# Optimization experiments

Hardware: AMD Instinct MI355X
Metric: run time of the kernel (lower is better)

The kernel has to match this reference:

```python
import jax, jax.numpy as jnp
import numpy as np

DIM = 1024
S_SIZE = 512
M_SIZE = 4096
L_SIZE = 8192
MERGE_THRESHOLD = 0.98
L_ALPHA = 0.1
K_PROMOTE = max(1, S_SIZE // 4)  # torch: min(len(candidates), max(1, s_size//4)); candidates >> s_size here


def _l2norm(x, axis=-1):
    # F.normalize(p=2) with eps clamp
    return x / jnp.maximum(jnp.linalg.norm(x, axis=axis, keepdims=True), 1e-12)


def _update(processed_tokens, s_memory, m_memory, l_memory, m_utility, l_utility, wq, bq, wk, bk, s_ptr):
    cand = processed_tokens.reshape(-1, DIM)
    # --- S tier: scatter top-k-norm candidates into ring buffer (vectorized; K<=S so slots distinct) ---
    norms = jnp.linalg.norm(cand, axis=1)
    _, top_idx = jax.lax.top_k(norms, K_PROMOTE)
    pos = (s_ptr + jnp.arange(K_PROMOTE)) % S_SIZE
    s_mem = s_memory.at[pos].set(cand[top_idx])
    s_ptr_new = (s_ptr + K_PROMOTE) % S_SIZE
    # --- promotion attention (1 head, only attn weights used): pick best short-term slot ---
    q = l_memory.mean(axis=0) @ wq.T + bq                      # [dim]
    kproj = s_mem @ wk.T + bk                                  # [S, dim]
    attn = jax.nn.softmax(kproj @ q / jnp.sqrt(jnp.asarray(DIM, cand.dtype)))
    best_s_idx = jnp.argmax(attn)
    candidate = s_mem[best_s_idx]                              # [dim]

    # --- M tier: promote / merge / replace ---
    def not_full(mm, mu):
        ridx = jnp.argmin(mu)
        return mm.at[ridx].set(candidate), mu.at[ridx].set(mu.mean() + 1e-5)

    def full(mm, mu):
        mm_norm = _l2norm(mm)
        sims = mm_norm @ _l2norm(candidate)                    # [M]
        msi = jnp.argmax(sims)
        sim_cand = sims[msi]

        def merge_with_candidate(mm, mu):
            merged = _l2norm((mm[msi] + candidate) / 2.0)
            return mm.at[msi].set(merged), mu.at[msi].set((mu[msi] + mu.mean()) / 2.0)

        def try_internal_merge(mm, mu):
            # most redundant pair: strict lower triangle of cosine sim matrix
            sim_mat = mm_norm @ mm_norm.T                      # [M, M]
            sim_mat = jnp.where(jnp.triu(jnp.ones((M_SIZE, M_SIZE), bool)), -1.0, sim_mat)
            flat = jnp.argmax(sim_mat)
            internal_sim = sim_mat.reshape(-1)[flat]
            idx1, idx2 = flat // M_SIZE, flat % M_SIZE

            def do_pair_merge(mm, mu):
                merged = _l2norm((mm[idx1] + mm[idx2]) / 2.0)
                mm2 = mm.at[idx1].set(merged).at[idx2].set(candidate)
                mu1 = mu.at[idx1].set((mu[idx1] + mu[idx2]) / 2.0)
                mu2 = mu1.at[idx2].set(mu1.mean() + 1e-5)      # torch recomputes mean after idx1 write
                return mm2, mu2

            def replace_weakest(mm, mu):
                li = jnp.argmin(mu)
                stronger = jnp.linalg.norm(candidate) > jnp.linalg.norm(mm[li])
                mm2 = jnp.where(stronger, mm.at[li].set(candidate), mm)
                mu2 = jnp.where(stronger, mu.at[li].set(mu.mean() + 1e-5), mu)
                return mm2, mu2

            return jax.lax.cond(internal_sim > MERGE_THRESHOLD, do_pair_merge, replace_weakest, mm, mu)

        return jax.lax.cond(sim_cand > MERGE_THRESHOLD, merge_with_candidate, try_internal_merge, mm, mu)

    is_m_full = ~jnp.any(m_utility == 0)
    m_mem, m_util = jax.lax.cond(is_m_full, full, not_full, m_memory, m_utility)
    # --- L tier: consolidate most-used M slot into least-used L slot ---
    mi = jnp.argmax(m_util)
    lj = jnp.argmin(l_utility)
    consolidated = (1.0 - L_ALPHA) * l_memory[lj] + L_ALPHA * m_mem[mi]
    l_mem = l_memory.at[lj].set(consolidated)
    l_util = l_utility.at[lj].set(l_utility.mean())            # mean of pre-write values
    return s_mem, m_mem, l_mem, m_util, l_util, s_ptr_new


def setup_inputs() -> dict:
    key = jax.random.key(0)
    ks = jax.random.split(key, 10)
    scale = 1.0 / np.sqrt(DIM)
    return {
        "processed_tokens": jax.random.normal(ks[0], (4, 4096, DIM), jnp.float32),
        "s_memory": jax.random.normal(ks[1], (S_SIZE, DIM), jnp.float32),
        "m_memory": jax.random.normal(ks[2], (M_SIZE, DIM), jnp.float32),
        "l_memory": jax.random.normal(ks[3], (L_SIZE, DIM), jnp.float32),
        "m_utility": jax.random.uniform(ks[4], (M_SIZE,), jnp.float32) + 0.01,  # >0 -> 'm full' branch
        "l_utility": jax.random.uniform(ks[5], (L_SIZE,), jnp.float32) + 0.01,
        "wq": jax.random.normal(ks[6], (DIM, DIM), jnp.float32) * scale,
        "bq": jnp.zeros((DIM,), jnp.float32),
        "wk": jax.random.normal(ks[7], (DIM, DIM), jnp.float32) * scale,
        "bk": jnp.zeros((DIM,), jnp.float32),
        "s_ptr": 0,
    }


def reference(processed_tokens, s_memory, m_memory, l_memory, m_utility, l_utility, wq, bq, wk, bk, s_ptr):
    return _update(processed_tokens, s_memory, m_memory, l_memory, m_utility, l_utility, wq, bq, wk, bk, s_ptr)
```

## Files before the change

### kernel.cpp

```cpp
#include <hip/hip_runtime.h>

#define DIMV 1024
#define SSZ 512
#define MSZ 4096
#define LSZ 8192
#define KPROM 128
#define NCAND 16384
#define NPAIR 528

typedef __attribute__((ext_vector_type(4))) float f32x4;
typedef __attribute__((ext_vector_type(4))) unsigned int u32x4;
typedef __attribute__((ext_vector_type(4))) unsigned short u16x4;
typedef __attribute__((ext_vector_type(8))) __bf16 bf16x8;

#define OUT_S 0ull
#define OUT_M 524288ull
#define OUT_L 4718592ull
#define OUT_MU 13107200ull
#define OUT_LU 13111296ull
#define OUT_SPTR 13119488ull

#define SCROWS 2080
#define SC_BF16 0ull
#define SC_NORMS 2097152ull
#define SC_TOPIDX 2113536ull
#define SC_RV 2113664ull
#define SC_LSUM 2114688ull
#define SC_QV 2115712ull
#define SC_LOGITS 2116736ull
#define SC_BEST 2117248ull
#define SC_MNORM 2117264ull
#define SC_SIMS 2121360ull
#define SC_PPV 2125456ull
#define SC_PPI 2125984ull

__device__ __forceinline__ float wave_sum(float v) {
#pragma unroll
  for (int o = 32; o > 0; o >>= 1) v += __shfl_down(v, o, 64);
  return v;
}
__device__ __forceinline__ void wave_maxidx(float& v, int& i) {
#pragma unroll
  for (int o = 32; o > 0; o >>= 1) {
    float ov = __shfl_down(v, o, 64);
    int oi = __shfl_down(i, o, 64);
    if (ov > v || (ov == v && oi < i)) { v = ov; i = oi; }
  }
}
__device__ __forceinline__ void wave_minidx(float& v, int& i) {
#pragma unroll
  for (int o = 32; o > 0; o >>= 1) {
    float ov = __shfl_down(v, o, 64);
    int oi = __shfl_down(i, o, 64);
    if (ov < v || (ov == v && oi < i)) { v = ov; i = oi; }
  }
}
__device__ __forceinline__ unsigned short f2bf(float x) {
  unsigned u = __float_as_uint(x);
  return (unsigned short)((u + 0x7FFFu + ((u >> 16) & 1u)) >> 16);
}
__device__ __forceinline__ void nts(f32x4* p, f32x4 v) { __builtin_nontemporal_store(v, p); }
__device__ __forceinline__ void gload16(const unsigned short* g, unsigned short* l) {
  __builtin_amdgcn_global_load_lds((const __attribute__((address_space(1))) unsigned int*)(g),
                                   (__attribute__((address_space(3))) unsigned int*)(l), 16, 0, 0);
}

__global__ void kA(const float* __restrict__ cand, const float* __restrict__ l_memory,
                   const float* __restrict__ m, float* __restrict__ norms,
                   float* __restrict__ lsum, unsigned short* __restrict__ mb,
                   float* __restrict__ mnorm, float* __restrict__ out_m,
                   float* __restrict__ out_l) {
  int b = blockIdx.x, t = threadIdx.x, lane = t & 63, w = t >> 6;
  if (b < 256) {
    int r0 = b * 32;
    const f32x4* base = (const f32x4*)l_memory + (size_t)r0 * 256;
    f32x4* dst = (f32x4*)out_l + (size_t)r0 * 256;
    bool wr = (r0 >= SCROWS);
    f32x4 a0 = {0.f, 0.f, 0.f, 0.f}, a1 = a0, a2 = a0, a3 = a0;
#pragma unroll 2
    for (int r = 0; r < 32; r += 4) {
      f32x4 v0 = base[(r + 0) * 256 + t];
      f32x4 v1 = base[(r + 1) * 256 + t];
      f32x4 v2 = base[(r + 2) * 256 + t];
      f32x4 v3 = base[(r + 3) * 256 + t];
      if (wr) {
        nts(&dst[(r + 0) * 256 + t], v0);
        nts(&dst[(r + 1) * 256 + t], v1);
        nts(&dst[(r + 2) * 256 + t], v2);
        nts(&dst[(r + 3) * 256 + t], v3);
      }
      a0 += v0; a1 += v1; a2 += v2; a3 += v3;
    }
    f32x4 a = (a0 + a1) + (a2 + a3);
    atomicAdd(&lsum[t * 4 + 0], a.x);
    atomicAdd(&lsum[t * 4 + 1], a.y);
    atomicAdd(&lsum[t * 4 + 2], a.z);
    atomicAdd(&lsum[t * 4 + 3], a.w);
  } else if (b < 512) {
    int r0 = (b - 256) * 16 + w * 4;
    const f32x4* base4 = (const f32x4*)(m + (size_t)r0 * DIMV);
    u16x4* mb4 = (u16x4*)(mb + (size_t)r0 * DIMV);
    f32x4* om4 = (f32x4*)(out_m + (size_t)r0 * DIMV);
    float s0 = 0.f, s1 = 0.f, s2 = 0.f, s3 = 0.f;
#pragma unroll
    for (int k = 0; k < 16; ++k) {
      int i = k * 64 + lane;
      f32x4 v = base4[i];
      float d = v.x * v.x + v.y * v.y + v.z * v.z + v.w * v.w;
      if (k < 4) s0 += d;
      else if (k < 8) s1 += d;
      else if (k < 12) s2 += d;
      else s3 += d;
      u16x4 h;
      h.x = f2bf(v.x); h.y = f2bf(v.y); h.z = f2bf(v.z); h.w = f2bf(v.w);
      mb4[i] = h;
      nts(&om4[i], v);
    }
    f32x4 sv = {s0, s1, s2, s3};
#pragma unroll
    for (int o = 32; o > 0; o >>= 1) {
      sv.x += __shfl_down(sv.x, o, 64);
      sv.y += __shfl_down(sv.y, o, 64);
      sv.z += __shfl_down(sv.z, o, 64);
      sv.w += __shfl_down(sv.w, o, 64);
    }
    if (lane == 0) {
      f32x4 o4 = {sqrtf(sv.x), sqrtf(sv.y), sqrtf(sv.z), sqrtf(sv.w)};
      *((f32x4*)(mnorm + r0)) = o4;
    }
  } else {
    int r0 = (b - 512) * 16 + w * 4;
    const f32x4* base4 = (const f32x4*)(cand + (size_t)r0 * DIMV);
    float s0 = 0.f, s1 = 0.f, s2 = 0.f, s3 = 0.f;
#pragma unroll
    for (int k = 0; k < 16; ++k) {
      f32x4 v = base4[k * 64 + lane];
      float d = v.x * v.x + v.y * v.y + v.z * v.z + v.w * v.w;
      if (k < 4) s0 += d;
      else if (k < 8) s1 += d;
      else if (k < 12) s2 += d;
      else s3 += d;
    }
    f32x4 sv = {s0, s1, s2, s3};
#pragma unroll
    for (int o = 32; o > 0; o >>= 1) {
      sv.x += __shfl_down(sv.x, o, 64);
      sv.y += __shfl_down(sv.y, o, 64);
      sv.z += __shfl_down(sv.z, o, 64);
      sv.w += __shfl_down(sv.w, o, 64);
    }
    if (lane == 0) {
      f32x4 o4 = {sqrtf(sv.x), sqrtf(sv.y), sqrtf(sv.z), sqrtf(sv.w)};
      *((f32x4*)(norms + r0)) = o4;
    }
  }
}

__device__ int scan_excl_1024(int v, int* sh, int* total) {
  int t = threadIdx.x;
  sh[t] = v;
  __syncthreads();
  for (int o = 1; o < 1024; o <<= 1) {
    int x = (t >= o) ? sh[t - o] : 0;
    __syncthreads();
    sh[t] += x;
    __syncthreads();
  }
  int incl = sh[t];
  *total = sh[1023];
  __syncthreads();
  return incl - v;
}

__global__ void kT(const float* __restrict__ norms, int* __restrict__ topidx) {
  int t = threadIdx.x;
  __shared__ int sh[1024];
  __shared__ int hist[256];
  __shared__ unsigned s_selkey[KPROM];
  __shared__ int s_selidx[KPROM];
  __shared__ int s_digit, s_sub;
  unsigned key[16];
  {
    const u32x4* np = (const u32x4*)norms;
    u32x4 k0 = np[t * 4 + 0], k1 = np[t * 4 + 1], k2 = np[t * 4 + 2], k3 = np[t * 4 + 3];
    key[0] = k0.x; key[1] = k0.y; key[2] = k0.z; key[3] = k0.w;
    key[4] = k1.x; key[5] = k1.y; key[6] = k1.z; key[7] = k1.w;
    key[8] = k2.x; key[9] = k2.y; key[10] = k2.z; key[11] = k2.w;
    key[12] = k3.x; key[13] = k3.y; key[14] = k3.z; key[15] = k3.w;
  }

  unsigned prefix = 0, himask = 0;
  int remaining = KPROM;
  for (int p = 24; p >= 0; p -= 8) {
    if (t < 256) hist[t] = 0;
    __syncthreads();
#pragma unroll
    for (int j = 0; j < 16; ++j)
      if ((key[j] & himask) == prefix) atomicAdd(&hist[(key[j] >> p) & 255], 1);
    __syncthreads();
    if (t < 256) sh[t] = hist[t];
    __syncthreads();
    for (int o = 1; o < 256; o <<= 1) {
      int x = (t < 256 && t + o < 256) ? sh[t + o] : 0;
      __syncthreads();
      if (t < 256) sh[t] += x;
      __syncthreads();
    }
    if (t < 256) {
      int sfex = (t < 255) ? sh[t + 1] : 0;
      if (sfex < remaining && remaining <= sh[t]) { s_digit = t; s_sub = sfex; }
    }
    __syncthreads();
    prefix |= ((unsigned)s_digit) << p;
    remaining -= s_sub;
    himask |= (0xFFu << p);
    __syncthreads();
  }
  unsigned T = prefix;

  int cgt = 0, ceq = 0;
#pragma unroll
  for (int j = 0; j < 16; ++j) { cgt += (key[j] > T); ceq += (key[j] == T); }
  int total_gt, total_eq;
  int sgt = scan_excl_1024(cgt, sh, &total_gt);
  int seq = scan_excl_1024(ceq, sh, &total_eq);
  int need_eq = KPROM - total_gt;
  int g = sgt, e = seq;
#pragma unroll
  for (int j = 0; j < 16; ++j) {
    if (key[j] > T) { s_selkey[g] = key[j]; s_selidx[g] = t * 16 + j; ++g; }
    else if (key[j] == T) {
      if (e < need_eq) { s_selkey[total_gt + e] = key[j]; s_selidx[total_gt + e] = t * 16 + j; }
      ++e;
    }
  }
  __syncthreads();
  if (t < KPROM) {
    unsigned mk = s_selkey[t];
    int mi = s_selidx[t];
    int rank = 0;
    for (int q2 = 0; q2 < KPROM; ++q2) {
      unsigned qk = s_selkey[q2];
      int qi = s_selidx[q2];
      rank += (qk > mk || (qk == mk && qi < mi)) ? 1 : 0;
    }
    topidx[rank] = mi;
  }
}

__global__ void kB(const float* __restrict__ cand, const float* __restrict__ s_memory,
                   const int* __restrict__ topidx, const int* __restrict__ s_ptr,
                   const float* __restrict__ wq, const float* __restrict__ bq,
                   const float* __restrict__ lsum, float* __restrict__ out_s,
                   float* __restrict__ out_sptr, float* __restrict__ qv) {
  int b = blockIdx.x, t = threadIdx.x;
  if (b < 512) {
    int sp = s_ptr[0];
    int k = (b - sp + SSZ) & (SSZ - 1);
    const float* src = (k < KPROM) ? (cand + (size_t)topidx[k] * DIMV) : (s_memory + (size_t)b * DIMV);
    ((f32x4*)(out_s + (size_t)b * DIMV))[t] = ((const f32x4*)src)[t];
    if (b == 0 && t == 0) out_sptr[0] = (float)((sp + KPROM) % SSZ);
  } else {
    int lane = t & 63, w = t >> 6;
    int d = (b - 512) * 4 + w;
    const f32x4* row = (const f32x4*)(wq + (size_t)d * DIMV);
    const f32x4* lm = (const f32x4*)lsum;
    float s = 0.f;
#pragma unroll
    for (int c = 0; c < 4; ++c) {
      f32x4 a = row[c * 64 + lane], bb = lm[c * 64 + lane];
      s += a.x * bb.x + a.y * bb.y + a.z * bb.z + a.w * bb.w;
    }
    s = wave_sum(s);
    if (lane == 0) qv[d] = s * (1.f / 8192.f) + bq[d];
  }
}

__global__ void kC(const float* __restrict__ wk, const float* __restrict__ qv,
                   float* __restrict__ rv) {
  int b = blockIdx.x, t = threadIdx.x;
  f32x4 a = {0.f, 0.f, 0.f, 0.f};
  for (int r = 0; r < 8; ++r) {
    float qd = qv[b * 8 + r];
    f32x4 v = ((const f32x4*)(wk + (size_t)(b * 8 + r) * DIMV))[t];
    a += v * qd;
  }
  atomicAdd(&rv[t * 4 + 0], a.x);
  atomicAdd(&rv[t * 4 + 1], a.y);
  atomicAdd(&rv[t * 4 + 2], a.z);
  atomicAdd(&rv[t * 4 + 3], a.w);
}

__global__ void kD(const float* __restrict__ out_s, const float* __restrict__ rv,
                   float* __restrict__ logits) {
  int lane = threadIdx.x & 63, w = threadIdx.x >> 6;
  int srow = blockIdx.x * 4 + w;
  const f32x4* a = (const f32x4*)(out_s + (size_t)srow * DIMV);
  const f32x4* b = (const f32x4*)rv;
  float s = 0.f;
#pragma unroll
  for (int c = 0; c < 4; ++c) {
    f32x4 x = a[c * 64 + lane], y = b[c * 64 + lane];
    s += x.x * y.x + x.y * y.y + x.z * y.z + x.w * y.w;
  }
  s = wave_sum(s);
  if (lane == 0) logits[srow] = s;
}

__global__ void kE(const float* __restrict__ logits, const float* __restrict__ out_s,
                   int* __restrict__ best, float* __restrict__ cnorm) {
  __shared__ float swv[4];
  __shared__ int swi[4];
  int t = threadIdx.x, lane = t & 63, w = t >> 6;
  float v0 = logits[t], v1 = logits[t + 256];
  float bv;
  int bidx;
  if (v1 > v0) { bv = v1; bidx = t + 256; } else { bv = v0; bidx = t; }
  wave_maxidx(bv, bidx);
  if (lane == 0) { swv[w] = bv; swi[w] = bidx; }
  __syncthreads();
  if (t == 0) {
    float a = swv[0]; int ai = swi[0];
    for (int i = 1; i < 4; ++i)
      if (swv[i] > a || (swv[i] == a && swi[i] < ai)) { a = swv[i]; ai = swi[i]; }
    best[0] = ai;
  }
  __syncthreads();
  int bi = best[0];
  f32x4 c4 = ((const f32x4*)(out_s + (size_t)bi * DIMV))[t];
  float s = c4.x * c4.x + c4.y * c4.y + c4.z * c4.z + c4.w * c4.w;
  s = wave_sum(s);
  __syncthreads();
  if (lane == 0) swv[w] = s;
  __syncthreads();
  if (t == 0) cnorm[0] = sqrtf(swv[0] + swv[1] + swv[2] + swv[3]);
}

__global__ __launch_bounds__(256, 3) void kG(const unsigned short* __restrict__ mb,
                                             const float* __restrict__ mnorm,
                                             const float* __restrict__ m,
                                             const float* __restrict__ out_s,
                                             const int* __restrict__ best,
                                             const float* __restrict__ cnorm,
                                             float* __restrict__ pv, int* __restrict__ pidx,
                                             float* __restrict__ sims) {
  int b = blockIdx.x, t = threadIdx.x, lane = t & 63, w = t >> 6;
  if (b >= NPAIR) {
    int row = (b - NPAIR) * 4 + w;
    const f32x4* mp = (const f32x4*)(m + (size_t)row * DIMV);
    const f32x4* cp = (const f32x4*)(out_s + (size_t)best[0] * DIMV);
    float sd = 0.f;
#pragma unroll
    for (int c = 0; c < 4; ++c) {
      int i = c * 64 + lane;
      f32x4 v = mp[i], u = cp[i];
      sd += v.x * u.x + v.y * u.y + v.z * u.z + v.w * u.w;
    }
    sd = wave_sum(sd);
    if (lane == 0) sims[row] = sd / (fmaxf(mnorm[row], 1e-12f) * fmaxf(cnorm[0], 1e-12f));
    return;
  }
  __shared__ unsigned short Ash[128 * 64];
  __shared__ unsigned short Bsh[128 * 64];
  __shared__ float spv[4];
  __shared__ int spi[4];

  int bs = (b & 7) * 66 + (b >> 3);
  int bi = (int)((sqrtf(8.f * (float)bs + 1.f) - 1.f) * 0.5f);
  while (bi * (bi + 1) / 2 > bs) --bi;
  while ((bi + 1) * (bi + 2) / 2 <= bs) ++bi;
  int bj = bs - bi * (bi + 1) / 2;
  int rowA0 = bi * 128, rowB0 = bj * 128;

  int wr = w >> 1, wc = w & 1;
  int rl = lane & 15, kq4 = lane >> 4;
  int swz = rl & 7;
  int subrow = lane >> 3, gg = lane & 7;
  int gsw = (gg ^ subrow) << 3;

  f32x4 acc[4][4];
  f32x4 z = {0.f, 0.f, 0.f, 0.f};
#pragma unroll
  for (int ti = 0; ti < 4; ++ti)
#pragma unroll
    for (int tj = 0; tj < 4; ++tj) acc[ti][tj] = z;

  for (int kc = 0; kc < DIMV; kc += 64) {
#pragma unroll
    for (int jj = 0; jj < 4; ++jj) {
      int rsub = w * 32 + jj * 8 + subrow;
      gload16(mb + (size_t)(rowA0 + rsub) * DIMV + kc + gsw, Ash + (w * 4 + jj) * 512);
      gload16(mb + (size_t)(rowB0 + rsub) * DIMV + kc + gsw, Bsh + (w * 4 + jj) * 512);
    }
    __syncthreads();
#pragma unroll
    for (int ks = 0; ks < 2; ++ks) {
      int co = (((ks * 4 + kq4) ^ swz) << 3);
      bf16x8 af[4], bfv[4];
#pragma unroll
      for (int ti = 0; ti < 4; ++ti)
        af[ti] = *(const bf16x8*)(Ash + (wr * 64 + ti * 16 + rl) * 64 + co);
#pragma unroll
      for (int tj = 0; tj < 4; ++tj)
        bfv[tj] = *(const bf16x8*)(Bsh + (wc * 64 + tj * 16 + rl) * 64 + co);
#pragma unroll
      for (int ti = 0; ti < 4; ++ti)
#pragma unroll
        for (int tj = 0; tj < 4; ++tj)
          acc[ti][tj] = __builtin_amdgcn_mfma_f32_16x16x32_bf16(af[ti], bfv[tj], acc[ti][tj], 0, 0, 0);
    }
    __syncthreads();
  }

  float ni[16], nj4[4];
#pragma unroll
  for (int ti = 0; ti < 4; ++ti)
#pragma unroll
    for (int r = 0; r < 4; ++r)
      ni[ti * 4 + r] = fmaxf(mnorm[rowA0 + wr * 64 + ti * 16 + kq4 * 4 + r], 1e-12f);
#pragma unroll
  for (int tj = 0; tj < 4; ++tj)
    nj4[tj] = fmaxf(mnorm[rowB0 + wc * 64 + tj * 16 + rl], 1e-12f);

  float bv = -3.402823466e38f;
  int bidx = 0x7FFFFFFF;
#pragma unroll
  for (int ti = 0; ti < 4; ++ti)
#pragma unroll
    for (int tj = 0; tj < 4; ++tj)
#pragma unroll
      for (int r = 0; r < 4; ++r) {
        int gi = rowA0 + wr * 64 + ti * 16 + kq4 * 4 + r;
        int gj = rowB0 + wc * 64 + tj * 16 + rl;
        if (gi > gj) {
          float s = acc[ti][tj][r] / (ni[ti * 4 + r] * nj4[tj]);
          int fi = gi * MSZ + gj;
          if (s > bv || (s == bv && fi < bidx)) { bv = s; bidx = fi; }
        }
      }
  wave_maxidx(bv, bidx);
  if (lane == 0) { spv[w] = bv; spi[w] = bidx; }
  __syncthreads();
  if (t == 0) {
    float a = spv[0]; int ai = spi[0];
    for (int i = 1; i < 4; ++i)
      if (spv[i] > a || (spv[i] == a && spi[i] < ai)) { a = spv[i]; ai = spi[i]; }
    pv[b] = a;
    pidx[b] = ai;
  }
}

__global__ void kH(const float* __restrict__ pv, const int* __restrict__ pidx,
                   const float* __restrict__ sims, const float* __restrict__ mu,
                   const float* __restrict__ mnorm, const float* __restrict__ cnorm,
                   const int* __restrict__ best, const float* __restrict__ lu,
                   float* __restrict__ out_mu, float* __restrict__ out_lu,
                   int* __restrict__ ws) {
  __shared__ float swv[16];
  __shared__ int swi[16];
  __shared__ float ssum[16];
  __shared__ int szf[16];
  __shared__ float s_res[2];
  __shared__ int s_resi[2];
  __shared__ int s_branch, s_i1, s_i2, s_lj;
  __shared__ float s_u1, s_u2, s_lmean;
  int t = threadIdx.x, lane = t & 63, w = t >> 6;

  float bv = -3.402823466e38f;
  int bidx = 0x7FFFFFFF;
  for (int i = t; i < NPAIR; i += 1024) {
    float v = pv[i];
    int fi = pidx[i];
    if (v > bv || (v == bv && fi < bidx)) { bv = v; bidx = fi; }
  }
  wave_maxidx(bv, bidx);
  if (lane == 0) { swv[w] = bv; swi[w] = bidx; }
  __syncthreads();
  if (t == 0) {
    float a = swv[0]; int ai = swi[0];
    for (int i = 1; i < 16; ++i)
      if (swv[i] > a || (swv[i] == a && swi[i] < ai)) { a = swv[i]; ai = swi[i]; }
    s_res[0] = a; s_resi[0] = ai;
  }
  __syncthreads();

  bv = -3.402823466e38f;
  bidx = 0x7FFFFFFF;
#pragma unroll
  for (int j = 0; j < 4; ++j) {
    int i = t * 4 + j;
    float v = sims[i];
    if (v > bv) { bv = v; bidx = i; }
  }
  wave_maxidx(bv, bidx);
  if (lane == 0) { swv[w] = bv; swi[w] = bidx; }
  __syncthreads();
  if (t == 0) {
    float a = swv[0]; int ai = swi[0];
    for (int i = 1; i < 16; ++i)
      if (swv[i] > a || (swv[i] == a && swi[i] < ai)) { a = swv[i]; ai = swi[i]; }
    s_res[1] = a; s_resi[1] = ai;
  }
  __syncthreads();

  float muv[4];
  float sum = 0.f, mnv = 3.402823466e38f;
  int mni = 0x7FFFFFFF, zf = 0;
#pragma unroll
  for (int j = 0; j < 4; ++j) {
    int i = t * 4 + j;
    float v = mu[i];
    muv[j] = v;
    sum += v;
    if (v < mnv) { mnv = v; mni = i; }
    if (v == 0.f) zf = 1;
  }
  sum = wave_sum(sum);
  wave_minidx(mnv, mni);
#pragma unroll
  for (int o = 32; o > 0; o >>= 1) zf |= __shfl_down(zf, o, 64);
  if (lane == 0) { ssum[w] = sum; swv[w] = mnv; swi[w] = mni; szf[w] = zf; }
  __syncthreads();
  if (t == 0) {
    float muSum = 0.f;
    int anyz = 0;
    float a = swv[0]; int li = swi[0];
    for (int i = 0; i < 16; ++i) {
      muSum += ssum[i];
      anyz |= szf[i];
      if (i > 0 && (swv[i] < a || (swv[i] == a && swi[i] < li))) { a = swv[i]; li = swi[i]; }
    }
    float muMean = muSum / 4096.f;
    float internal_sim = s_res[0];
    int iflat = s_resi[0];
    float sim_cand = s_res[1];
    int msi = s_resi[1];
    int branch, i1 = -1, i2 = -1;
    float u1 = 0.f, u2 = 0.f;
    if (anyz) {
      branch = 0; i1 = li; u1 = muMean + 1e-5f;
    } else if (sim_cand > 0.98f) {
      branch = 1; i1 = msi; u1 = (mu[msi] + muMean) * 0.5f;
    } else if (internal_sim > 0.98f) {
      branch = 2; i1 = iflat / MSZ; i2 = iflat - (iflat / MSZ) * MSZ;
      float o1 = mu[i1], o2 = mu[i2];
      u1 = (o1 + o2) * 0.5f;
      u2 = (muSum - o1 + u1) / 4096.f + 1e-5f;
    } else {
      if (cnorm[0] > mnorm[li]) { branch = 0; i1 = li; u1 = muMean + 1e-5f; }
      else branch = 4;
    }
    s_branch = branch; s_i1 = i1; s_i2 = i2; s_u1 = u1; s_u2 = u2;
    ws[2] = branch; ws[3] = i1; ws[4] = i2; ws[5] = best[0];
  }
  __syncthreads();

  int branch = s_branch, i1 = s_i1, i2 = s_i2;
  float u1 = s_u1, u2 = s_u2;
  bv = -3.402823466e38f;
  bidx = 0x7FFFFFFF;
#pragma unroll
  for (int j = 0; j < 4; ++j) {
    int i = t * 4 + j;
    float v = muv[j];
    if (branch != 4 && i == i1) v = u1;
    if (branch == 2 && i == i2) v = u2;
    out_mu[i] = v;
    if (v > bv) { bv = v; bidx = i; }
  }
  wave_maxidx(bv, bidx);
  __syncthreads();
  if (lane == 0) { swv[w] = bv; swi[w] = bidx; }
  __syncthreads();
  if (t == 0) {
    float a = swv[0]; int ai = swi[0];
    for (int i = 1; i < 16; ++i)
      if (swv[i] > a || (swv[i] == a && swi[i] < ai)) { a = swv[i]; ai = swi[i]; }
    ws[1] = ai;
  }

  float luv[8];
  sum = 0.f; mnv = 3.402823466e38f; mni = 0x7FFFFFFF;
#pragma unroll
  for (int j = 0; j < 8; ++j) {
    int i = t * 8 + j;
    float v = lu[i];
    luv[j] = v;
    sum += v;
    if (v < mnv) { mnv = v; mni = i; }
  }
  sum = wave_sum(sum);
  wave_minidx(mnv, mni);
  __syncthreads();
  if (lane == 0) { swv[w] = mnv; swi[w] = mni; ssum[w] = sum; }
  __syncthreads();
  if (t == 0) {
    float a = swv[0]; int ai = swi[0];
    float ls = 0.f;
    for (int i = 0; i < 16; ++i) {
      ls += ssum[i];
      if (i > 0 && (swv[i] < a || (swv[i] == a && swi[i] < ai))) { a = swv[i]; ai = swi[i]; }
    }
    s_lj = ai;
    s_lmean = ls / 8192.f;
    ws[0] = ai;
  }
  __syncthreads();
  int lj = s_lj;
  float lmv = s_lmean;
#pragma unroll
  for (int j = 0; j < 8; ++j) {
    int i = t * 8 + j;
    out_lu[i] = (i == lj) ? lmv : luv[j];
  }
}

__global__ void kI(const float* __restrict__ m, const float* __restrict__ l_memory,
                   const float* __restrict__ out_s, const int* __restrict__ ws,
                   float* __restrict__ out_m, float* __restrict__ out_l) {
  __shared__ float sred[4];
  int b = blockIdx.x, t = threadIdx.x, lane = t & 63, w = t >> 6;
  int lj = ws[0], mi = ws[1], branch = ws[2], i1 = ws[3], i2 = ws[4], best = ws[5];
  if (b < 520) {
    int r0 = b * 4;
    const f32x4* src = (const f32x4*)(l_memory + (size_t)r0 * DIMV);
    f32x4* dst = (f32x4*)(out_l + (size_t)r0 * DIMV);
#pragma unroll
    for (int k = 0; k < 4; ++k) {
      if (r0 + k == lj) continue;
      nts(&dst[k * 256 + t], src[k * 256 + t]);
    }
    return;
  }
  if (b == 520) {
    if (branch == 4) return;
    int row = i1;
    f32x4* dst = (f32x4*)(out_m + (size_t)row * DIMV);
    if (branch == 0) {
      dst[t] = ((const f32x4*)(out_s + (size_t)best * DIMV))[t];
    } else {
      f32x4 a = ((const f32x4*)(m + (size_t)row * DIMV))[t];
      f32x4 bb = (branch == 1) ? ((const f32x4*)(out_s + (size_t)best * DIMV))[t]
                               : ((const f32x4*)(m + (size_t)i2 * DIMV))[t];
      f32x4 v = (a + bb) * 0.5f;
      float ss = v.x * v.x + v.y * v.y + v.z * v.z + v.w * v.w;
      ss = wave_sum(ss);
      if (lane == 0) sred[w] = ss;
      __syncthreads();
      float nrm = fmaxf(sqrtf(sred[0] + sred[1] + sred[2] + sred[3]), 1e-12f);
      dst[t] = v / nrm;
    }
    return;
  }
  if (b == 521) {
    if (branch != 2) return;
    ((f32x4*)(out_m + (size_t)i2 * DIMV))[t] = ((const f32x4*)(out_s + (size_t)best * DIMV))[t];
    return;
  }
  f32x4 v = ((const f32x4*)(l_memory + (size_t)lj * DIMV))[t];
  int mode = 0;
  if ((branch == 0 && mi == i1) || (branch == 2 && mi == i2)) mode = 1;
  else if (branch == 1 && mi == i1) mode = 2;
  else if (branch == 2 && mi == i1) mode = 3;
  f32x4 mv;
  if (mode == 0) {
    mv = ((const f32x4*)(m + (size_t)mi * DIMV))[t];
  } else if (mode == 1) {
    mv = ((const f32x4*)(out_s + (size_t)best * DIMV))[t];
  } else {
    f32x4 a = ((const f32x4*)(m + (size_t)mi * DIMV))[t];
    f32x4 bb = (mode == 2) ? ((const f32x4*)(out_s + (size_t)best * DIMV))[t]
                           : ((const f32x4*)(m + (size_t)i2 * DIMV))[t];
    f32x4 vm = (a + bb) * 0.5f;
    float ss = vm.x * vm.x + vm.y * vm.y + vm.z * vm.z + vm.w * vm.w;
    ss = wave_sum(ss);
    if (lane == 0) sred[w] = ss;
    __syncthreads();
    float nrm = fmaxf(sqrtf(sred[0] + sred[1] + sred[2] + sred[3]), 1e-12f);
    mv = vm / nrm;
  }
  v = v * 0.9f + mv * 0.1f;
  ((f32x4*)(out_l + (size_t)lj * DIMV))[t] = v;
}

extern "C" void kernel_launch(void* const* d_in, const int* in_sizes, int n_in,
                              void* d_out, int out_size, void* d_ws, size_t ws_size,
                              hipStream_t stream) {
  const float* cand = (const float*)d_in[0];
  const float* s_memory = (const float*)d_in[1];
  const float* m_memory = (const float*)d_in[2];
  const float* l_memory = (const float*)d_in[3];
  const float* m_utility = (const float*)d_in[4];
  const float* l_utility = (const float*)d_in[5];
  const float* wq = (const float*)d_in[6];
  const float* bq = (const float*)d_in[7];
  const float* wk = (const float*)d_in[8];
  const float* bk = (const float*)d_in[9];
  const int* s_ptr = (const int*)d_in[10];
  (void)bk;

  float* out = (float*)d_out;
  float* out_s = out + OUT_S;
  float* out_m = out + OUT_M;
  float* out_l = out + OUT_L;
  float* out_mu = out + OUT_MU;
  float* out_lu = out + OUT_LU;
  float* out_sptr = out + OUT_SPTR;

  float* lsc = out_l;
  unsigned short* mb = (unsigned short*)(lsc + SC_BF16);
  float* norms = lsc + SC_NORMS;
  int* topidx = (int*)(lsc + SC_TOPIDX);
  float* rv = lsc + SC_RV;
  float* lsum = lsc + SC_LSUM;
  float* qv = lsc + SC_QV;
  float* logits = lsc + SC_LOGITS;
  int* best = (int*)(lsc + SC_BEST);
  float* cnorm = lsc + SC_BEST + 1;
  float* mnorm = lsc + SC_MNORM;
  float* sims = lsc + SC_SIMS;
  float* pv = lsc + SC_PPV;
  int* pidx = (int*)(lsc + SC_PPI);
  int* wsctl = (int*)d_ws;

  hipMemsetAsync(rv, 0, 8192, stream);
  kA<<<1536, 256, 0, stream>>>(cand, l_memory, m_memory, norms, lsum, mb, mnorm, out_m, out_l);
  kT<<<1, 1024, 0, stream>>>(norms, topidx);
  kB<<<768, 256, 0, stream>>>(cand, s_memory, topidx, s_ptr, wq, bq, lsum, out_s, out_sptr, qv);
  kC<<<128, 256, 0, stream>>>(wk, qv, rv);
  kD<<<128, 256, 0, stream>>>(out_s, rv, logits);
  kE<<<1, 256, 0, stream>>>(logits, out_s, best, cnorm);
  kG<<<NPAIR + 1024, 256, 0, stream>>>(mb, mnorm, m_memory, out_s, best, cnorm, pv, pidx, sims);
  kH<<<1, 1024, 0, stream>>>(pv, pidx, sims, m_utility, mnorm, cnorm, best, l_utility,
                             out_mu, out_lu, wsctl);
  kI<<<523, 256, 0, stream>>>(m_memory, l_memory, out_s, wsctl, out_m, out_l);
}
```

Measured before the change: 294.2 us.

## Fuse promotion-attention kernels into one persistent kernel with grid barriers

Replaces the kB/kC/kD/kE chain and the memset with a single 256-block kernel that uses a software grid barrier between phases. The L-memory column sum now goes to per-block partial sums reduced inside the fused kernel, instead of atomics. Non-temporal stores are switched to plain stores. The scratch region grows, so kI copies more rows. The aim is to cut launch gaps and atomic contention, at the cost of spin-wait barriers that depend on all 256 blocks being co-resident.

After: 370.3 us. +25.9%, slower.

```diff
diff --git a/kernel.cpp b/kernel.cpp
--- a/kernel.cpp
+++ b/kernel.cpp
@@ -7,6 +7,7 @@
 #define KPROM 128
 #define NCAND 16384
 #define NPAIR 528
+#define QNB 256
 
 typedef __attribute__((ext_vector_type(4))) float f32x4;
 typedef __attribute__((ext_vector_type(4))) unsigned int u32x4;
@@ -20,19 +21,19 @@
 #define OUT_LU 13111296ull
 #define OUT_SPTR 13119488ull
 
-#define SCROWS 2080
+#define SCROWS 2336
 #define SC_BF16 0ull
 #define SC_NORMS 2097152ull
 #define SC_TOPIDX 2113536ull
-#define SC_RV 2113664ull
-#define SC_LSUM 2114688ull
-#define SC_QV 2115712ull
-#define SC_LOGITS 2116736ull
-#define SC_BEST 2117248ull
-#define SC_MNORM 2117264ull
-#define SC_SIMS 2121360ull
-#define SC_PPV 2125456ull
-#define SC_PPI 2125984ull
+#define SC_LPART 2113664ull
+#define SC_LMEAN 2375808ull
+#define SC_RV 2376832ull
+#define SC_LOGITS 2377856ull
+#define SC_BEST 2378368ull
+#define SC_MNORM 2378372ull
+#define SC_SIMS 2382468ull
+#define SC_PPV 2386564ull
+#define SC_PPI 2387092ull
 
 __device__ __forceinline__ float wave_sum(float v) {
 #pragma unroll
@@ -59,18 +60,36 @@
   unsigned u = __float_as_uint(x);
   return (unsigned short)((u + 0x7FFFu + ((u >> 16) & 1u)) >> 16);
 }
-__device__ __forceinline__ void nts(f32x4* p, f32x4 v) { __builtin_nontemporal_store(v, p); }
 __device__ __forceinline__ void gload16(const unsigned short* g, unsigned short* l) {
   __builtin_amdgcn_global_load_lds((const __attribute__((address_space(1))) unsigned int*)(g),
                                    (__attribute__((address_space(3))) unsigned int*)(l), 16, 0, 0);
 }
+__device__ __forceinline__ void gbar(int* cnt, int* gen) {
+  __syncthreads();
+  if (threadIdx.x == 0) {
+    __threadfence();
+    int g0 = __hip_atomic_load(gen, __ATOMIC_RELAXED, __HIP_MEMORY_SCOPE_AGENT);
+    int a = __hip_atomic_fetch_add(cnt, 1, __ATOMIC_ACQ_REL, __HIP_MEMORY_SCOPE_AGENT);
+    if (a == QNB - 1) {
+      __hip_atomic_store(cnt, 0, __ATOMIC_RELAXED, __HIP_MEMORY_SCOPE_AGENT);
+      __threadfence();
+      __hip_atomic_fetch_add(gen, 1, __ATOMIC_ACQ_REL, __HIP_MEMORY_SCOPE_AGENT);
+    } else {
+      while (__hip_atomic_load(gen, __ATOMIC_RELAXED, __HIP_MEMORY_SCOPE_AGENT) == g0)
+        __builtin_amdgcn_s_sleep(2);
+    }
+    __threadfence();
+  }
+  __syncthreads();
+}
 
 __global__ void kA(const float* __restrict__ cand, const float* __restrict__ l_memory,
                    const float* __restrict__ m, float* __restrict__ norms,
-                   float* __restrict__ lsum, unsigned short* __restrict__ mb,
+                   float* __restrict__ lpart, unsigned short* __restrict__ mb,
                    float* __restrict__ mnorm, float* __restrict__ out_m,
-                   float* __restrict__ out_l) {
+                   float* __restrict__ out_l, int* __restrict__ bar) {
   int b = blockIdx.x, t = threadIdx.x, lane = t & 63, w = t >> 6;
+  if (b == 0 && t == 0) bar[0] = 0;
   if (b < 256) {
     int r0 = b * 32;
     const f32x4* base = (const f32x4*)l_memory + (size_t)r0 * 256;
@@ -84,18 +103,15 @@
       f32x4 v2 = base[(r + 2) * 256 + t];
       f32x4 v3 = base[(r + 3) * 256 + t];
       if (wr) {
-        nts(&dst[(r + 0) * 256 + t], v0);
-        nts(&dst[(r + 1) * 256 + t], v1);
-        nts(&dst[(r + 2) * 256 + t], v2);
-        nts(&dst[(r + 3) * 256 + t], v3);
+        dst[(r + 0) * 256 + t] = v0;
+        dst[(r + 1) * 256 + t] = v1;
+        dst[(r + 2) * 256 + t] = v2;
+        dst[(r + 3) * 256 + t] = v3;
       }
       a0 += v0; a1 += v1; a2 += v2; a3 += v3;
     }
     f32x4 a = (a0 + a1) + (a2 + a3);
-    atomicAdd(&lsum[t * 4 + 0], a.x);
-    atomicAdd(&lsum[t * 4 + 1], a.y);
-    atomicAdd(&lsum[t * 4 + 2], a.z);
-    atomicAdd(&lsum[t * 4 + 3], a.w);
+    ((f32x4*)(lpart + (size_t)b * DIMV))[t] = a;
   } else if (b < 512) {
     int r0 = (b - 256) * 16 + w * 4;
     const f32x4* base4 = (const f32x4*)(m + (size_t)r0 * DIMV);
@@ -114,7 +130,7 @@
       u16x4 h;
       h.x = f2bf(v.x); h.y = f2bf(v.y); h.z = f2bf(v.z); h.w = f2bf(v.w);
       mb4[i] = h;
-      nts(&om4[i], v);
+      om4[i] = v;
     }
     f32x4 sv = {s0, s1, s2, s3};
 #pragma unroll
@@ -248,23 +264,55 @@
   }
 }
 
-__global__ void kB(const float* __restrict__ cand, const float* __restrict__ s_memory,
-                   const int* __restrict__ topidx, const int* __restrict__ s_ptr,
-                   const float* __restrict__ wq, const float* __restrict__ bq,
-                   const float* __restrict__ lsum, float* __restrict__ out_s,
-                   float* __restrict__ out_sptr, float* __restrict__ qv) {
-  int b = blockIdx.x, t = threadIdx.x;
-  if (b < 512) {
+__global__ __launch_bounds__(256) void kQ(const float* __restrict__ cand,
+                                          const float* __restrict__ s_memory,
+                                          const int* __restrict__ topidx,
+                                          const int* __restrict__ s_ptr,
+                                          const float* __restrict__ wq,
+                                          const float* __restrict__ bq,
+                                          const float* __restrict__ wk,
+                                          const float* __restrict__ lpart,
+                                          float* __restrict__ lmean, float* __restrict__ rv,
+                                          float* __restrict__ logits, float* __restrict__ out_s,
+                                          float* __restrict__ out_sptr, int* __restrict__ best,
+                                          float* __restrict__ cnorm, int* __restrict__ bar) {
+  int b = blockIdx.x, t = threadIdx.x, lane = t & 63, w = t >> 6;
+  __shared__ f32x4 red4[256];
+  __shared__ float qs[4];
+  __shared__ float swv[4];
+  __shared__ int swi[4];
+
+  {
+    f32x4 v = *(const f32x4*)(lpart + (size_t)t * DIMV + b * 4);
+    red4[t] = v;
+    __syncthreads();
+    for (int o = 128; o > 0; o >>= 1) {
+      if (t < o) red4[t] += red4[t + o];
+      __syncthreads();
+    }
+    if (t == 0) {
+      f32x4 r = red4[0] * (1.f / 8192.f);
+      *(f32x4*)(lmean + b * 4) = r;
+      f32x4 z = {0.f, 0.f, 0.f, 0.f};
+      *(f32x4*)(rv + b * 4) = z;
+    }
     int sp = s_ptr[0];
-    int k = (b - sp + SSZ) & (SSZ - 1);
-    const float* src = (k < KPROM) ? (cand + (size_t)topidx[k] * DIMV) : (s_memory + (size_t)b * DIMV);
-    ((f32x4*)(out_s + (size_t)b * DIMV))[t] = ((const f32x4*)src)[t];
     if (b == 0 && t == 0) out_sptr[0] = (float)((sp + KPROM) % SSZ);
-  } else {
-    int lane = t & 63, w = t >> 6;
-    int d = (b - 512) * 4 + w;
+#pragma unroll
+    for (int k = 0; k < 2; ++k) {
+      int row = b * 2 + k;
+      int ki = (row - sp + SSZ) & (SSZ - 1);
+      const float* src =
+          (ki < KPROM) ? (cand + (size_t)topidx[ki] * DIMV) : (s_memory + (size_t)row * DIMV);
+      ((f32x4*)(out_s + (size_t)row * DIMV))[t] = ((const f32x4*)src)[t];
+    }
+  }
+  gbar(&bar[0], &bar[1]);
+
+  {
+    int d = b * 4 + w;
     const f32x4* row = (const f32x4*)(wq + (size_t)d * DIMV);
-    const f32x4* lm = (const f32x4*)lsum;
+    const f32x4* lm = (const f32x4*)lmean;
     float s = 0.f;
 #pragma unroll
     for (int c = 0; c < 4; ++c) {
@@ -272,68 +320,63 @@
       s += a.x * bb.x + a.y * bb.y + a.z * bb.z + a.w * bb.w;
     }
     s = wave_sum(s);
-    if (lane == 0) qv[d] = s * (1.f / 8192.f) + bq[d];
-  }
-}
-
-__global__ void kC(const float* __restrict__ wk, const float* __restrict__ qv,
-                   float* __restrict__ rv) {
-  int b = blockIdx.x, t = threadIdx.x;
-  f32x4 a = {0.f, 0.f, 0.f, 0.f};
-  for (int r = 0; r < 8; ++r) {
-    float qd = qv[b * 8 + r];
-    f32x4 v = ((const f32x4*)(wk + (size_t)(b * 8 + r) * DIMV))[t];
-    a += v * qd;
-  }
-  atomicAdd(&rv[t * 4 + 0], a.x);
-  atomicAdd(&rv[t * 4 + 1], a.y);
-  atomicAdd(&rv[t * 4 + 2], a.z);
-  atomicAdd(&rv[t * 4 + 3], a.w);
-}
-
-__global__ void kD(const float* __restrict__ out_s, const float* __restrict__ rv,
-                   float* __restrict__ logits) {
-  int lane = threadIdx.x & 63, w = threadIdx.x >> 6;
-  int srow = blockIdx.x * 4 + w;
-  const f32x4* a = (const f32x4*)(out_s + (size_t)srow * DIMV);
-  const f32x4* b = (const f32x4*)rv;
-  float s = 0.f;
-#pragma unroll
-  for (int c = 0; c < 4; ++c) {
-    f32x4 x = a[c * 64 + lane], y = b[c * 64 + lane];
-    s += x.x * y.x + x.y * y.y + x.z * y.z + x.w * y.w;
-  }
-  s = wave_sum(s);
-  if (lane == 0) logits[srow] = s;
-}
-
-__global__ void kE(const float* __restrict__ logits, const float* __restrict__ out_s,
-                   int* __restrict__ best, float* __restrict__ cnorm) {
-  __shared__ float swv[4];
-  __shared__ int swi[4];
-  int t = threadIdx.x, lane = t & 63, w = t >> 6;
-  float v0 = logits[t], v1 = logits[t + 256];
-  float bv;
-  int bidx;
-  if (v1 > v0) { bv = v1; bidx = t + 256; } else { bv = v0; bidx = t; }
-  wave_maxidx(bv, bidx);
-  if (lane == 0) { swv[w] = bv; swi[w] = bidx; }
-  __syncthreads();
-  if (t == 0) {
-    float a = swv[0]; int ai = swi[0];
-    for (int i = 1; i < 4; ++i)
-      if (swv[i] > a || (swv[i] == a && swi[i] < ai)) { a = swv[i]; ai = swi[i]; }
-    best[0] = ai;
-  }
-  __syncthreads();
-  int bi = best[0];
-  f32x4 c4 = ((const f32x4*)(out_s + (size_t)bi * DIMV))[t];
-  float s = c4.x * c4.x + c4.y * c4.y + c4.z * c4.z + c4.w * c4.w;
-  s = wave_sum(s);
-  __syncthreads();
-  if (lane == 0) swv[w] = s;
-  __syncthreads();
-  if (t == 0) cnorm[0] = sqrtf(swv[0] + swv[1] + swv[2] + swv[3]);
+    if (lane == 0) qs[w] = s + bq[d];
+  }
+  __syncthreads();
+  {
+    f32x4 a = {0.f, 0.f, 0.f, 0.f};
+#pragma unroll
+    for (int r = 0; r < 4; ++r) {
+      float qd = qs[r];
+      f32x4 v = ((const f32x4*)(wk + (size_t)(b * 4 + r) * DIMV))[t];
+      a += v * qd;
+    }
+    atomicAdd(&rv[t * 4 + 0], a.x);
+    atomicAdd(&rv[t * 4 + 1], a.y);
+    atomicAdd(&rv[t * 4 + 2], a.z);
+    atomicAdd(&rv[t * 4 + 3], a.w);
+  }
+  gbar(&bar[0], &bar[1]);
+
+  if (w < 2) {
+    int srow = b * 2 + w;
+    const f32x4* a4 = (const f32x4*)(out_s + (size_t)srow * DIMV);
+    const f32x4* r4 = (const f32x4*)rv;
+    float s = 0.f;
+#pragma unroll
+    for (int c = 0; c < 4; ++c) {
+      f32x4 x = a4[c * 64 + lane], y = r4[c * 64 + lane];
+      s += x.x * y.x + x.y * y.y + x.z * y.z + x.w * y.w;
+    }
+    s = wave_sum(s);
+    if (lane == 0) logits[srow] = s;
+  }
+  gbar(&bar[0], &bar[1]);
+
+  if (b == 0) {
+    float v0 = logits[t], v1 = logits[t + 256];
+    float bv;
+    int bidx;
+    if (v1 > v0) { bv = v1; bidx = t + 256; } else { bv = v0; bidx = t; }
+    wave_maxidx(bv, bidx);
+    if (lane == 0) { swv[w] = bv; swi[w] = bidx; }
+    __syncthreads();
+    if (t == 0) {
+      float a = swv[0]; int ai = swi[0];
+      for (int i = 1; i < 4; ++i)
+        if (swv[i] > a || (swv[i] == a && swi[i] < ai)) { a = swv[i]; ai = swi[i]; }
+      best[0] = ai;
+    }
+    __syncthreads();
+    int bi = best[0];
+    f32x4 c4 = ((const f32x4*)(out_s + (size_t)bi * DIMV))[t];
+    float s = c4.x * c4.x + c4.y * c4.y + c4.z * c4.z + c4.w * c4.w;
+    s = wave_sum(s);
+    __syncthreads();
+    if (lane == 0) swv[w] = s;
+    __syncthreads();
+    if (t == 0) cnorm[0] = sqrtf(swv[0] + swv[1] + swv[2] + swv[3]);
+  }
 }
 
 __global__ __launch_bounds__(256, 3) void kG(const unsigned short* __restrict__ mb,
@@ -621,18 +664,18 @@
   __shared__ float sred[4];
   int b = blockIdx.x, t = threadIdx.x, lane = t & 63, w = t >> 6;
   int lj = ws[0], mi = ws[1], branch = ws[2], i1 = ws[3], i2 = ws[4], best = ws[5];
-  if (b < 520) {
+  if (b < 584) {
     int r0 = b * 4;
     const f32x4* src = (const f32x4*)(l_memory + (size_t)r0 * DIMV);
     f32x4* dst = (f32x4*)(out_l + (size_t)r0 * DIMV);
 #pragma unroll
     for (int k = 0; k < 4; ++k) {
       if (r0 + k == lj) continue;
-      nts(&dst[k * 256 + t], src[k * 256 + t]);
+      dst[k * 256 + t] = src[k * 256 + t];
     }
     return;
   }
-  if (b == 520) {
+  if (b == 584) {
     if (branch == 4) return;
     int row = i1;
     f32x4* dst = (f32x4*)(out_m + (size_t)row * DIMV);
@@ -652,7 +695,7 @@
     }
     return;
   }
-  if (b == 521) {
+  if (b == 585) {
     if (branch != 2) return;
     ((f32x4*)(out_m + (size_t)i2 * DIMV))[t] = ((const f32x4*)(out_s + (size_t)best * DIMV))[t];
     return;
@@ -711,9 +754,9 @@
   unsigned short* mb = (unsigned short*)(lsc + SC_BF16);
   float* norms = lsc + SC_NORMS;
   int* topidx = (int*)(lsc + SC_TOPIDX);
+  float* lpart = lsc + SC_LPART;
+  float* lmean = lsc + SC_LMEAN;
   float* rv = lsc + SC_RV;
-  float* lsum = lsc + SC_LSUM;
-  float* qv = lsc + SC_QV;
   float* logits = lsc + SC_LOGITS;
   int* best = (int*)(lsc + SC_BEST);
   float* cnorm = lsc + SC_BEST + 1;
@@ -723,15 +766,13 @@
   int* pidx = (int*)(lsc + SC_PPI);
   int* wsctl = (int*)d_ws;
 
-  hipMemsetAsync(rv, 0, 8192, stream);
-  kA<<<1536, 256, 0, stream>>>(cand, l_memory, m_memory, norms, lsum, mb, mnorm, out_m, out_l);
+  kA<<<1536, 256, 0, stream>>>(cand, l_memory, m_memory, norms, lpart, mb, mnorm, out_m, out_l,
+                               wsctl + 8);
   kT<<<1, 1024, 0, stream>>>(norms, topidx);
-  kB<<<768, 256, 0, stream>>>(cand, s_memory, topidx, s_ptr, wq, bq, lsum, out_s, out_sptr, qv);
-  kC<<<128, 256, 0, stream>>>(wk, qv, rv);
-  kD<<<128, 256, 0, stream>>>(out_s, rv, logits);
-  kE<<<1, 256, 0, stream>>>(logits, out_s, best, cnorm);
+  kQ<<<QNB, 256, 0, stream>>>(cand, s_memory, topidx, s_ptr, wq, bq, wk, lpart, lmean, rv, logits,
+                              out_s, out_sptr, best, cnorm, wsctl + 8);
   kG<<<NPAIR + 1024, 256, 0, stream>>>(mb, mnorm, m_memory, out_s, best, cnorm, pv, pidx, sims);
-  kH<<<1, 1024, 0, stream>>>(pv, pidx, sims, m_utility, mnorm, cnorm, best, l_utility,
-                             out_mu, out_lu, wsctl);
-  kI<<<523, 256, 0, stream>>>(m_memory, l_memory, out_s, wsctl, out_m, out_l);
-}
+  kH<<<1, 1024, 0, stream>>>(pv, pidx, sims, m_utility, mnorm, cnorm, best, l_utility, out_mu,
+                             out_lu, wsctl);
+  kI<<<587, 256, 0, stream>>>(m_memory, l_memory, out_s, wsctl, out_m, out_l);
+}
```
